# Optimization experiments

Hardware: AMD Instinct MI355X
Metric: run time of the kernel (lower is better)

## Reference

```python
import jax, jax.numpy as jnp
import numpy as np

D_MODEL = 1024
N_HEADS = 16
D_HEAD = D_MODEL // N_HEADS
B, L = 4, 2048
NEG_INF = float('-inf')


def setup_inputs() -> dict:
    key = jax.random.key(0)
    ks = jax.random.split(key, 8)
    x = jax.random.normal(ks[0], (B, L, D_MODEL), dtype=jnp.float32)
    # sorted cumulative event times in hours (~0-2000h span)
    timestamps = jnp.cumsum(jax.random.uniform(ks[1], (B, L), dtype=jnp.float32), axis=-1)
    mask = jnp.ones((B, L), dtype=jnp.float32)
    s = 1.0 / np.sqrt(D_MODEL)
    W_qkv = jax.random.normal(ks[2], (3 * D_MODEL, D_MODEL), dtype=jnp.float32) * s
    b_qkv = jnp.zeros((3 * D_MODEL,), dtype=jnp.float32)
    W_out = jax.random.normal(ks[3], (D_MODEL, D_MODEL), dtype=jnp.float32) * s
    b_out = jnp.zeros((D_MODEL,), dtype=jnp.float32)
    decay_rate = jnp.full((N_HEADS,), 0.01, dtype=jnp.float32)
    return {"x": x, "timestamps": timestamps, "mask": mask,
            "W_qkv": W_qkv, "b_qkv": b_qkv, "W_out": W_out, "b_out": b_out,
            "decay_rate": decay_rate}


def reference(x, timestamps, mask, W_qkv, b_qkv, W_out, b_out, decay_rate):
    Bb, Ll, Dd = x.shape
    H, dh = N_HEADS, D_HEAD
    scale = dh ** (-0.5)
    qkv = x @ W_qkv.T + b_qkv                     # (B,L,3D)
    qkv = qkv.reshape(Bb, Ll, 3, H, dh).transpose(2, 0, 3, 1, 4)  # (3,B,H,L,dh)
    q, k, v = qkv[0], qkv[1], qkv[2]
    attn = jnp.einsum('bhqd,bhkd->bhqk', q, k) * scale
    t_diff = jnp.abs(timestamps[:, :, None] - timestamps[:, None, :])[:, None]  # (B,1,L,L)
    decay = jax.nn.softplus(decay_rate)[None, :, None, None]                    # (1,H,1,1)
    attn = attn - decay * t_diff / 24.0
    causal = jnp.triu(jnp.ones((Ll, Ll), dtype=bool), k=1)        # (L,L) True above diag
    attn = jnp.where(causal[None, None], NEG_INF, attn)
    pad = (mask == 0.0)[:, None, None, :]                         # (B,1,1,L) True=pad key
    attn = jnp.where(pad, NEG_INF, attn)
    attn = jax.nn.softmax(attn, axis=-1)
    out = jnp.einsum('bhqk,bhkd->bhqd', attn, v)                  # (B,H,L,dh)
    out = out.transpose(0, 2, 1, 3).reshape(Bb, Ll, Dd)
    return out @ W_out.T + b_out
```

## Files before the change

### kernel.cpp

```cpp
#include <hip/hip_runtime.h>
#include <stdint.h>
#include <math.h>

#define B_   4
#define L_   2048
#define H_   16
#define DH_  64
#define DM_  1024

typedef __bf16 bf16;
typedef __attribute__((ext_vector_type(8))) __bf16 bf16x8;
typedef __attribute__((ext_vector_type(4))) float f32x4;
typedef __attribute__((ext_vector_type(4))) int i32x4;
typedef __attribute__((ext_vector_type(4))) short s16x4;
typedef unsigned short u16;
typedef unsigned int u32;
typedef __attribute__((ext_vector_type(2))) unsigned int u32x2;
typedef __attribute__((ext_vector_type(4))) unsigned short u16x4;

typedef unsigned int u32g __attribute__((address_space(1)));
typedef unsigned int u32l __attribute__((address_space(3)));

__device__ __forceinline__ u16 f2bf(float f) {
  return __builtin_bit_cast(u16, (bf16)f);
}

__device__ __forceinline__ float exp2_fast(float x) {
  float r; asm("v_exp_f32 %0, %1" : "=v"(r) : "v"(x)); return r;
}

__device__ __forceinline__ void gload16(const void* g, void* l) {
  __builtin_amdgcn_global_load_lds((const u32g*)g, (u32l*)l, 16, 0, 0);
}

__device__ __forceinline__ f32x4 mfma16(s16x4 a, s16x4 b, f32x4 c) {
#if __has_builtin(__builtin_amdgcn_mfma_f32_16x16x16bf16_1k)
  return __builtin_amdgcn_mfma_f32_16x16x16bf16_1k(a, b, c, 0, 0, 0);
#else
  asm volatile("v_mfma_f32_16x16x16_bf16 %0, %1, %2, %0\n\ts_nop 7\n\ts_nop 2"
               : "+v"(c) : "v"(a), "v"(b));
  return c;
#endif
}

#define NX4 2097152
#define NQ4 786432
#define NO4 262144
__global__ __launch_bounds__(256) void cvt3(const float* __restrict__ x,
                                            const float* __restrict__ wq,
                                            const float* __restrict__ wo,
                                            u16* __restrict__ xb, u16* __restrict__ wqb,
                                            u16* __restrict__ wob) {
  int i = blockIdx.x * 256 + threadIdx.x;
  const float* src; u16* dst; int j;
  if (i < NX4)            { src = x;  dst = xb;  j = i; }
  else if (i < NX4 + NQ4) { src = wq; dst = wqb; j = i - NX4; }
  else                    { src = wo; dst = wob; j = i - NX4 - NQ4; }
  f32x4 v = ((const f32x4*)src)[j];
  u16x4 o;
  o[0] = f2bf(v[0]); o[1] = f2bf(v[1]); o[2] = f2bf(v[2]); o[3] = f2bf(v[3]);
  ((u16x4*)dst)[j] = o;
}

__global__ __launch_bounds__(256) void bias_fill(const float* __restrict__ ts,
                                                 const float* __restrict__ msk,
                                                 const float* __restrict__ decay,
                                                 float* __restrict__ Bk) {
  int i = blockIdx.x * 256 + threadIdx.x;
  int bh = i >> 11, l = i & (L_ - 1);
  int b = bh >> 4, h = bh & 15;
  float dc24 = log1pf(__expf(decay[h])) * (1.0f / 24.0f) * 1.44269504f;
  float tv = ts[b * L_ + l], mv = msk[b * L_ + l];
  Bk[i] = (mv != 0.f) ? dc24 * tv : -INFINITY;
}

__global__ __launch_bounds__(512) void gemm_bf16(
    const u16* __restrict__ A, const u16* __restrict__ Bm, const float* __restrict__ bias,
    int M, int N, int K, int mode,
    u16* __restrict__ Qb, u16* __restrict__ Kb, u16* __restrict__ Vt, float* __restrict__ Cout)
{
  __shared__ char smem[147456];
  u16* ltr = (u16*)smem;

  const int tid = threadIdx.x;
  const int nwg = gridDim.x;
  int idx = blockIdx.x;
  idx = (idx & 7) * (nwg >> 3) + (idx >> 3);
  const int nbx = N >> 7;
  const int bx = idx % nbx, by = idx / nbx;
  const int m0 = by << 8, n0 = bx << 7;

  const int lane = tid & 63, w = tid >> 6;
  const int g = lane >> 4, col = lane & 15;
  const int wr = w >> 1, wc = w & 1;

  f32x4 acc[4][4];
#pragma unroll
  for (int mt = 0; mt < 4; ++mt)
#pragma unroll
    for (int nt = 0; nt < 4; ++nt) {
      acc[mt][nt][0] = 0.f; acc[mt][nt][1] = 0.f;
      acc[mt][nt][2] = 0.f; acc[mt][nt][3] = 0.f;
    }

  auto STAGE_A = [&](int kt, int nb, int hh) {
    char* dA = smem + nb * 49152;
    const int k0 = kt << 6;
#pragma unroll
    for (int pp = hh * 2; pp < hh * 2 + 2; ++pp) {
      int c = tid + pp * 512;
      int row = c >> 3, cc = c & 7;
      gload16(A + (size_t)(m0 + row) * K + k0 + ((cc ^ (row & 7)) << 3), dA + c * 16);
    }
  };
  auto STAGE_B = [&](int kt, int nb) {
    char* dB = smem + nb * 49152 + 32768;
    const int k0 = kt << 6;
#pragma unroll
    for (int pp = 0; pp < 2; ++pp) {
      int c = tid + pp * 512;
      int row = c >> 3, cc = c & 7;
      gload16(Bm + (size_t)(n0 + row) * K + k0 + ((cc ^ (row & 7)) << 3), dB + c * 16);
    }
  };

  STAGE_A(0, 0, 0); STAGE_A(0, 0, 1); STAGE_B(0, 0);
  STAGE_A(1, 1, 0); STAGE_A(1, 1, 1); STAGE_B(1, 1);
  asm volatile("s_waitcnt vmcnt(6)" ::: "memory");
  __builtin_amdgcn_s_barrier();

  const int nk = K >> 6;
  for (int t = 0; t < nk; ++t) {
    const char* bufA = smem + (t % 3) * 49152;
    const char* bufB = bufA + 32768;
    const bool pf = (t + 2 < nk);
    const int nb2 = (t + 2) % 3;

    bf16x8 af[4][2], bfr[4][2];
    auto RDA = [&](int mt, int kk) {
      int row = wr * 64 + mt * 16 + col;
      return *(const bf16x8*)(bufA + row * 128 + ((((kk << 2) + g) ^ (row & 7)) << 4));
    };
    auto RDB = [&](int nt, int kk) {
      int row = wc * 64 + nt * 16 + col;
      return *(const bf16x8*)(bufB + row * 128 + ((((kk << 2) + g) ^ (row & 7)) << 4));
    };
    auto QUAD = [&](int qm, int qn) {
      __builtin_amdgcn_s_setprio(1);
#pragma unroll
      for (int mi = 0; mi < 2; ++mi)
#pragma unroll
        for (int ni = 0; ni < 2; ++ni)
#pragma unroll
          for (int kk = 0; kk < 2; ++kk)
            acc[qm * 2 + mi][qn * 2 + ni] = __builtin_amdgcn_mfma_f32_16x16x32_bf16(
                af[qm * 2 + mi][kk], bfr[qn * 2 + ni][kk], acc[qm * 2 + mi][qn * 2 + ni], 0, 0, 0);
      __builtin_amdgcn_s_setprio(0);
    };

#pragma unroll
    for (int mi = 0; mi < 2; ++mi) { af[mi][0] = RDA(mi, 0); af[mi][1] = RDA(mi, 1); }
#pragma unroll
    for (int ni = 0; ni < 2; ++ni) { bfr[ni][0] = RDB(ni, 0); bfr[ni][1] = RDB(ni, 1); }
    if (pf) STAGE_A(t + 2, nb2, 0);
    __builtin_amdgcn_s_barrier();
    asm volatile("s_waitcnt lgkmcnt(0)" ::: "memory");
    __builtin_amdgcn_sched_barrier(0);
    QUAD(0, 0);
    __builtin_amdgcn_s_barrier();

#pragma unroll
    for (int ni = 2; ni < 4; ++ni) { bfr[ni][0] = RDB(ni, 0); bfr[ni][1] = RDB(ni, 1); }
    if (pf) STAGE_A(t + 2, nb2, 1);
    __builtin_amdgcn_s_barrier();
    asm volatile("s_waitcnt lgkmcnt(0)" ::: "memory");
    __builtin_amdgcn_sched_barrier(0);
    QUAD(0, 1);
    __builtin_amdgcn_s_barrier();

#pragma unroll
    for (int mi = 2; mi < 4; ++mi) { af[mi][0] = RDA(mi, 0); af[mi][1] = RDA(mi, 1); }
    if (pf) STAGE_B(t + 2, nb2);
    __builtin_amdgcn_s_barrier();
    asm volatile("s_waitcnt lgkmcnt(0)" ::: "memory");
    __builtin_amdgcn_sched_barrier(0);
    QUAD(1, 1);
    __builtin_amdgcn_s_barrier();

    QUAD(1, 0);
    if (pf)              asm volatile("s_waitcnt vmcnt(6)" ::: "memory");
    else if (t + 1 < nk) asm volatile("s_waitcnt vmcnt(0)" ::: "memory");
    __builtin_amdgcn_s_barrier();
  }

  if (mode == 1) {
#pragma unroll
    for (int nt = 0; nt < 4; ++nt) {
      int gn = n0 + wc * 64 + nt * 16 + col;
      float bv = bias[gn];
#pragma unroll
      for (int mt = 0; mt < 4; ++mt) {
        int mbase = m0 + wr * 64 + mt * 16 + g * 4;
#pragma unroll
        for (int r = 0; r < 4; ++r)
          Cout[(size_t)(mbase + r) * N + gn] = acc[mt][nt][r] + bv;
      }
    }
    return;
  }

  const int type = n0 >> 10;
  const float qsc = (type == 0) ? 0.125f * 1.44269504f : 1.0f;
#pragma unroll
  for (int nt = 0; nt < 4; ++nt) {
    int nn = wc * 64 + nt * 16 + col;
    float bv = bias[n0 + nn];
#pragma unroll
    for (int mt = 0; mt < 4; ++mt) {
      int mm = wr * 64 + mt * 16 + g * 4;
#pragma unroll
      for (int r = 0; r < 4; ++r) {
        u16 hv = f2bf((acc[mt][nt][r] + bv) * qsc);
        if (type < 2) ltr[(mm + r) * 136 + nn] = hv;
        else          ltr[nn * 264 + (mm + r)] = hv;
      }
    }
  }
  __syncthreads();
  if (type < 2) {
#pragma unroll
    for (int it = 0; it < 8; ++it) {
      int cid = tid + it * 512;
      int rrow = cid >> 4, cc = cid & 15;
      i32x4 v = *(const i32x4*)((const char*)ltr + rrow * 272 + cc * 16);
      int token = m0 + rrow;
      int bb = token >> 11, ll = token & (L_ - 1);
      int gn = n0 + cc * 8;
      int head = (gn & 1023) >> 6, d = gn & 63;
      u16* dst = (type == 0) ? Qb : Kb;
      *(i32x4*)(dst + ((size_t)((bb * H_ + head) * L_ + ll)) * 64 + d) = v;
    }
  } else {
#pragma unroll
    for (int it = 0; it < 8; ++it) {
      int cid = tid + it * 512;
      int rrow = cid >> 5, cc = cid & 31;
      i32x4 v = *(const i32x4*)((const char*)ltr + rrow * 528 + cc * 16);
      int gn = n0 + rrow;
      int head = (gn & 1023) >> 6, d = gn & 63;
      int token0 = m0 + cc * 8;
      int bb = token0 >> 11, ll = token0 & (L_ - 1);
      *(i32x4*)(Vt + ((size_t)((bb * H_ + head) * DH_ + d)) * L_ + ll) = v;
    }
  }
}

__global__ __launch_bounds__(512, 2) void attn_fwd(
    const u16* __restrict__ Qb, const u16* __restrict__ Kb, const u16* __restrict__ Vt,
    const float* __restrict__ Bk, u16* __restrict__ AO)
{
  __shared__ u16 lK[3][64 * 64];
  __shared__ u16 lV[3][64 * 64];

  const int phys = blockIdx.x;
  const int xcd = phys & 7, s = phys >> 3;
  const int bh = xcd * 8 + (s >> 3);
  const int pr = s & 7;
  const int qa = pr, qbt = 15 - pr;
  const int b = bh >> 4, h = bh & 15;

  const int tid = threadIdx.x, w = tid >> 6, lane = tid & 63;
  const int g = lane >> 4, q16 = lane & 15;

  const float* Bkb = Bk + (size_t)bh * L_;

  int kcol[2], vcol[4];
#pragma unroll
  for (int kk = 0; kk < 2; ++kk) kcol[kk] = ((kk * 4 + g) ^ (q16 & 7)) << 4;
#pragma unroll
  for (int t = 0; t < 4; ++t)
    vcol[t] = (((2 * t + (g >> 1)) ^ (q16 & 7)) << 4) + (g & 1) * 8;

  const int nkA = (qa + 1) * 2;
  const int nkB = (qbt + 1) * 2;

  auto STAGE = [&](int gst, int nb) {
    const int kt = (gst < nkA) ? gst : gst - nkA;
    const int kg0 = kt * 64;
    const int r8 = tid >> 3, cc = tid & 7;
    gload16(Kb + ((size_t)bh * L_ + kg0 + r8) * 64 + ((cc ^ (r8 & 7)) * 8),
            (char*)lK[nb] + tid * 16);
    gload16(Vt + ((size_t)(bh * 64 + r8)) * L_ + kg0 + ((cc ^ (r8 & 7)) * 8),
            (char*)lV[nb] + tid * 16);
  };

  auto BODY = [&](bf16x8 (&qf)[2], f32x4 (&o)[4], float& l_r, float mn,
                  int qrow, int kg0, int cur) {
    f32x4 sv[4];
#pragma unroll
    for (int t = 0; t < 4; ++t)
      sv[t] = *(const f32x4*)(Bkb + kg0 + t * 16 + g * 4);

    __builtin_amdgcn_s_setprio(1);
#pragma unroll
    for (int t = 0; t < 4; ++t) {
      const char* krow = (const char*)lK[cur] + t * 2048 + q16 * 128;
#pragma unroll
      for (int kk = 0; kk < 2; ++kk) {
        bf16x8 kf = *(const bf16x8*)(krow + kcol[kk]);
        sv[t] = __builtin_amdgcn_mfma_f32_16x16x32_bf16(kf, qf[kk], sv[t], 0, 0, 0);
      }
    }
    __builtin_amdgcn_s_setprio(0);

    if (kg0 + 63 > qrow) {
      const int qg = qrow + q16;
#pragma unroll
      for (int t = 0; t < 4; ++t)
#pragma unroll
        for (int r = 0; r < 4; ++r)
          sv[t][r] = (kg0 + t * 16 + g * 4 + r <= qg) ? sv[t][r] : -INFINITY;
    }

    float rs = 0.f;
#pragma unroll
    for (int t = 0; t < 4; ++t)
#pragma unroll
      for (int r = 0; r < 4; ++r) {
        float pv = exp2_fast(sv[t][r] - mn);
        sv[t][r] = pv;
        rs += pv;
      }
    l_r += rs;

    s16x4 pf[4];
#pragma unroll
    for (int t = 0; t < 4; ++t) {
      s16x4 pp;
      pp[0] = (short)f2bf(sv[t][0]); pp[1] = (short)f2bf(sv[t][1]);
      pp[2] = (short)f2bf(sv[t][2]); pp[3] = (short)f2bf(sv[t][3]);
      pf[t] = pp;
    }

    __builtin_amdgcn_s_setprio(1);
#pragma unroll
    for (int t = 0; t < 4; ++t) {
      const char* vrow = (const char*)lV[cur] + q16 * 128 + vcol[t];
#pragma unroll
      for (int db = 0; db < 4; ++db) {
        s16x4 vf = *(const s16x4*)(vrow + db * 2048);
        o[db] = mfma16(vf, pf[t], o[db]);
      }
    }
    __builtin_amdgcn_s_setprio(0);
  };

  auto EPI = [&](f32x4 (&o)[4], float l_r, int qt) {
    float lt = l_r + __shfl_xor(l_r, 16);
    lt += __shfl_xor(lt, 32);
    float inv = 1.f / lt;
    u16* dst = AO + ((size_t)(b * L_ + qt * 128 + w * 16 + q16)) * DM_ + h * 64 + g * 4;
#pragma unroll
    for (int db = 0; db < 4; ++db) {
      u32x2 pk;
      pk[0] = (u32)f2bf(o[db][0] * inv) | ((u32)f2bf(o[db][1] * inv) << 16);
      pk[1] = (u32)f2bf(o[db][2] * inv) | ((u32)f2bf(o[db][3] * inv) << 16);
      *(u32x2*)(dst + db * 16) = pk;
    }
  };

  STAGE(0, 0);
  STAGE(1, 1);
  asm volatile("s_waitcnt vmcnt(2) lgkmcnt(0)" ::: "memory");
  __builtin_amdgcn_s_barrier();
  __builtin_amdgcn_sched_barrier(0);

  {
    const int qrow = qa * 128 + w * 16;
    const int mkt = (qrow + 79) >> 6;
    const float mn = Bkb[qrow + q16] + 8.f;
    bf16x8 qf[2];
    {
      const u16* Qr = Qb + ((size_t)bh * L_ + qrow + q16) * 64;
      qf[0] = *(const bf16x8*)(Qr + g * 8);
      qf[1] = *(const bf16x8*)(Qr + 32 + g * 8);
    }
    float l_r = 0.f;
    f32x4 o[4];
#pragma unroll
    for (int db = 0; db < 4; ++db) {
      o[db][0] = 0.f; o[db][1] = 0.f; o[db][2] = 0.f; o[db][3] = 0.f;
    }
    for (int st = 0; st < nkA; ++st) {
      const int cur = st % 3;
      STAGE(st + 2, (st + 2) % 3);
      if (st < mkt) BODY(qf, o, l_r, mn, qrow, st * 64, cur);
      asm volatile("s_waitcnt vmcnt(2) lgkmcnt(0)" ::: "memory");
      __builtin_amdgcn_s_barrier();
      __builtin_amdgcn_sched_barrier(0);
    }
    EPI(o, l_r, qa);
  }

  {
    const int qrow = qbt * 128 + w * 16;
    const int mkt = (qrow + 79) >> 6;
    const float mn = Bkb[qrow + q16] + 8.f;
    bf16x8 qf[2];
    {
      const u16* Qr = Qb + ((size_t)bh * L_ + qrow + q16) * 64;
      qf[0] = *(const bf16x8*)(Qr + g * 8);
      qf[1] = *(const bf16x8*)(Qr + 32 + g * 8);
    }
    float l_r = 0.f;
    f32x4 o[4];
#pragma unroll
    for (int db = 0; db < 4; ++db) {
      o[db][0] = 0.f; o[db][1] = 0.f; o[db][2] = 0.f; o[db][3] = 0.f;
    }
    for (int kt = 0; kt < nkB; ++kt) {
      const int gst = nkA + kt;
      const int cur = gst % 3;
      const bool pf = (kt + 2 < nkB);
      if (pf) STAGE(gst + 2, (gst + 2) % 3);
      if (kt < mkt) BODY(qf, o, l_r, mn, qrow, kt * 64, cur);
      if (kt + 1 < nkB) {
        if (pf) asm volatile("s_waitcnt vmcnt(2) lgkmcnt(0)" ::: "memory");
        else    asm volatile("s_waitcnt vmcnt(0) lgkmcnt(0)" ::: "memory");
        __builtin_amdgcn_s_barrier();
        __builtin_amdgcn_sched_barrier(0);
      }
    }
    EPI(o, l_r, qbt);
  }
}

extern "C" void kernel_launch(void* const* d_in, const int* in_sizes, int n_in,
                              void* d_out, int out_size, void* d_ws, size_t ws_size,
                              hipStream_t stream) {
  const float* x    = (const float*)d_in[0];
  const float* ts   = (const float*)d_in[1];
  const float* mk   = (const float*)d_in[2];
  const float* Wqkv = (const float*)d_in[3];
  const float* bqkv = (const float*)d_in[4];
  const float* Wout = (const float*)d_in[5];
  const float* bout = (const float*)d_in[6];
  const float* dec  = (const float*)d_in[7];
  float* out = (float*)d_out;

  char* ws = (char*)d_ws;
  u16* xbf  = (u16*)(ws + 0);
  u16* wqbf = (u16*)(ws + 16777216);
  u16* wobf = (u16*)(ws + 23068672);
  u16* Qb   = (u16*)(ws + 25165824);
  u16* Kb   = (u16*)(ws + 41943040);
  u16* Vt   = (u16*)(ws + 58720256);
  u16* AO   = (u16*)(ws + 75497472);
  float* Bk = (float*)(ws + 92274688);

  cvt3<<<dim3((NX4 + NQ4 + NO4) / 256), 256, 0, stream>>>(x, Wqkv, Wout, xbf, wqbf, wobf);

  bias_fill<<<dim3(64 * 2048 / 256), 256, 0, stream>>>(ts, mk, dec, Bk);

  gemm_bf16<<<dim3(768), 512, 0, stream>>>(
      xbf, wqbf, bqkv, 8192, 3072, 1024, 0, Qb, Kb, Vt, nullptr);

  attn_fwd<<<dim3(512), 512, 0, stream>>>(Qb, Kb, Vt, Bk, AO);

  gemm_bf16<<<dim3(256), 512, 0, stream>>>(
      AO, wobf, bout, 8192, 1024, 1024, 1, nullptr, nullptr, nullptr, out);
}
```

Baseline: 184.1 us.

## Share K/V tiles between paired query tiles in one fused loop

The kernel used to process two query tiles (qa and 15-qa) one after the other, loading the K/V tiles for the qa range twice. The loop is now merged, so each staged K/V tile feeds both query tiles' QK and PV MFMAs while the shorter tile is active. This cuts global loads and barriers for the overlapping range. In exchange it doubles accumulator and score registers, which may lower occupancy or cause spills.

```diff
diff --git a/kernel.cpp b/kernel.cpp
--- a/kernel.cpp
+++ b/kernel.cpp
@@ -284,8 +284,31 @@
   const int nkA = (qa + 1) * 2;
   const int nkB = (qbt + 1) * 2;
 
-  auto STAGE = [&](int gst, int nb) {
-    const int kt = (gst < nkA) ? gst : gst - nkA;
+  const int qrowA = qa * 128 + w * 16, qrowB = qbt * 128 + w * 16;
+  const int mktA = (qrowA + 79) >> 6;
+  const int mktB = (qrowB + 79) >> 6;
+  const float mnA = Bkb[qrowA + q16] + 8.f;
+  const float mnB = Bkb[qrowB + q16] + 8.f;
+
+  bf16x8 qfA[2], qfB[2];
+  {
+    const u16* Qr = Qb + ((size_t)bh * L_ + qrowA + q16) * 64;
+    qfA[0] = *(const bf16x8*)(Qr + g * 8);
+    qfA[1] = *(const bf16x8*)(Qr + 32 + g * 8);
+    Qr = Qb + ((size_t)bh * L_ + qrowB + q16) * 64;
+    qfB[0] = *(const bf16x8*)(Qr + g * 8);
+    qfB[1] = *(const bf16x8*)(Qr + 32 + g * 8);
+  }
+
+  float lA = 0.f, lB = 0.f;
+  f32x4 oA[4], oB[4];
+#pragma unroll
+  for (int db = 0; db < 4; ++db) {
+    oA[db][0] = 0.f; oA[db][1] = 0.f; oA[db][2] = 0.f; oA[db][3] = 0.f;
+    oB[db][0] = 0.f; oB[db][1] = 0.f; oB[db][2] = 0.f; oB[db][3] = 0.f;
+  }
+
+  auto STAGE = [&](int kt, int nb) {
     const int kg0 = kt * 64;
     const int r8 = tid >> 3, cc = tid & 7;
     gload16(Kb + ((size_t)bh * L_ + kg0 + r8) * 64 + ((cc ^ (r8 & 7)) * 8),
@@ -294,12 +317,15 @@
             (char*)lV[nb] + tid * 16);
   };
 
-  auto BODY = [&](bf16x8 (&qf)[2], f32x4 (&o)[4], float& l_r, float mn,
-                  int qrow, int kg0, int cur) {
-    f32x4 sv[4];
+  auto BODY = [&](bool doA, int kg0, int cur) {
+    f32x4 bk[4];
 #pragma unroll
     for (int t = 0; t < 4; ++t)
-      sv[t] = *(const f32x4*)(Bkb + kg0 + t * 16 + g * 4);
+      bk[t] = *(const f32x4*)(Bkb + kg0 + t * 16 + g * 4);
+
+    f32x4 svA[4], svB[4];
+#pragma unroll
+    for (int t = 0; t < 4; ++t) { if (doA) svA[t] = bk[t]; svB[t] = bk[t]; }
 
     __builtin_amdgcn_s_setprio(1);
 #pragma unroll
@@ -308,38 +334,59 @@
 #pragma unroll
       for (int kk = 0; kk < 2; ++kk) {
         bf16x8 kf = *(const bf16x8*)(krow + kcol[kk]);
-        sv[t] = __builtin_amdgcn_mfma_f32_16x16x32_bf16(kf, qf[kk], sv[t], 0, 0, 0);
+        if (doA) svA[t] = __builtin_amdgcn_mfma_f32_16x16x32_bf16(kf, qfA[kk], svA[t], 0, 0, 0);
+        svB[t] = __builtin_amdgcn_mfma_f32_16x16x32_bf16(kf, qfB[kk], svB[t], 0, 0, 0);
       }
     }
     __builtin_amdgcn_s_setprio(0);
 
-    if (kg0 + 63 > qrow) {
-      const int qg = qrow + q16;
+    if (doA && kg0 + 63 > qrowA) {
+      const int qg = qrowA + q16;
 #pragma unroll
       for (int t = 0; t < 4; ++t)
 #pragma unroll
         for (int r = 0; r < 4; ++r)
-          sv[t][r] = (kg0 + t * 16 + g * 4 + r <= qg) ? sv[t][r] : -INFINITY;
-    }
-
-    float rs = 0.f;
-#pragma unroll
-    for (int t = 0; t < 4; ++t)
-#pragma unroll
-      for (int r = 0; r < 4; ++r) {
-        float pv = exp2_fast(sv[t][r] - mn);
-        sv[t][r] = pv;
-        rs += pv;
-      }
-    l_r += rs;
-
-    s16x4 pf[4];
-#pragma unroll
-    for (int t = 0; t < 4; ++t) {
-      s16x4 pp;
-      pp[0] = (short)f2bf(sv[t][0]); pp[1] = (short)f2bf(sv[t][1]);
-      pp[2] = (short)f2bf(sv[t][2]); pp[3] = (short)f2bf(sv[t][3]);
-      pf[t] = pp;
+          svA[t][r] = (kg0 + t * 16 + g * 4 + r <= qg) ? svA[t][r] : -INFINITY;
+    }
+    if (kg0 + 63 > qrowB) {
+      const int qg = qrowB + q16;
+#pragma unroll
+      for (int t = 0; t < 4; ++t)
+#pragma unroll
+        for (int r = 0; r < 4; ++r)
+          svB[t][r] = (kg0 + t * 16 + g * 4 + r <= qg) ? svB[t][r] : -INFINITY;
+    }
+
+    s16x4 pfA[4], pfB[4];
+    if (doA) {
+      float rs = 0.f;
+#pragma unroll
+      for (int t = 0; t < 4; ++t) {
+        s16x4 pp;
+#pragma unroll
+        for (int r = 0; r < 4; ++r) {
+          float pv = exp2_fast(svA[t][r] - mnA);
+          rs += pv;
+          pp[r] = (short)f2bf(pv);
+        }
+        pfA[t] = pp;
+      }
+      lA += rs;
+    }
+    {
+      float rs = 0.f;
+#pragma unroll
+      for (int t = 0; t < 4; ++t) {
+        s16x4 pp;
+#pragma unroll
+        for (int r = 0; r < 4; ++r) {
+          float pv = exp2_fast(svB[t][r] - mnB);
+          rs += pv;
+          pp[r] = (short)f2bf(pv);
+        }
+        pfB[t] = pp;
+      }
+      lB += rs;
     }
 
     __builtin_amdgcn_s_setprio(1);
@@ -349,7 +396,8 @@
 #pragma unroll
       for (int db = 0; db < 4; ++db) {
         s16x4 vf = *(const s16x4*)(vrow + db * 2048);
-        o[db] = mfma16(vf, pf[t], o[db]);
+        if (doA) oA[db] = mfma16(vf, pfA[t], oA[db]);
+        oB[db] = mfma16(vf, pfB[t], oB[db]);
       }
     }
     __builtin_amdgcn_s_setprio(0);
@@ -375,64 +423,21 @@
   __builtin_amdgcn_s_barrier();
   __builtin_amdgcn_sched_barrier(0);
 
-  {
-    const int qrow = qa * 128 + w * 16;
-    const int mkt = (qrow + 79) >> 6;
-    const float mn = Bkb[qrow + q16] + 8.f;
-    bf16x8 qf[2];
-    {
-      const u16* Qr = Qb + ((size_t)bh * L_ + qrow + q16) * 64;
-      qf[0] = *(const bf16x8*)(Qr + g * 8);
-      qf[1] = *(const bf16x8*)(Qr + 32 + g * 8);
-    }
-    float l_r = 0.f;
-    f32x4 o[4];
-#pragma unroll
-    for (int db = 0; db < 4; ++db) {
-      o[db][0] = 0.f; o[db][1] = 0.f; o[db][2] = 0.f; o[db][3] = 0.f;
-    }
-    for (int st = 0; st < nkA; ++st) {
-      const int cur = st % 3;
-      STAGE(st + 2, (st + 2) % 3);
-      if (st < mkt) BODY(qf, o, l_r, mn, qrow, st * 64, cur);
-      asm volatile("s_waitcnt vmcnt(2) lgkmcnt(0)" ::: "memory");
+  for (int kt = 0; kt < nkB; ++kt) {
+    const int cur = kt % 3;
+    const bool pf = (kt + 2 < nkB);
+    if (pf) STAGE(kt + 2, (kt + 2) % 3);
+    if (kt < mktA)      BODY(true,  kt * 64, cur);
+    else if (kt < mktB) BODY(false, kt * 64, cur);
+    if (kt + 1 < nkB) {
+      if (pf) asm volatile("s_waitcnt vmcnt(2) lgkmcnt(0)" ::: "memory");
+      else    asm volatile("s_waitcnt vmcnt(0) lgkmcnt(0)" ::: "memory");
       __builtin_amdgcn_s_barrier();
       __builtin_amdgcn_sched_barrier(0);
     }
-    EPI(o, l_r, qa);
-  }
-
-  {
-    const int qrow = qbt * 128 + w * 16;
-    const int mkt = (qrow + 79) >> 6;
-    const float mn = Bkb[qrow + q16] + 8.f;
-    bf16x8 qf[2];
-    {
-      const u16* Qr = Qb + ((size_t)bh * L_ + qrow + q16) * 64;
-      qf[0] = *(const bf16x8*)(Qr + g * 8);
-      qf[1] = *(const bf16x8*)(Qr + 32 + g * 8);
-    }
-    float l_r = 0.f;
-    f32x4 o[4];
-#pragma unroll
-    for (int db = 0; db < 4; ++db) {
-      o[db][0] = 0.f; o[db][1] = 0.f; o[db][2] = 0.f; o[db][3] = 0.f;
-    }
-    for (int kt = 0; kt < nkB; ++kt) {
-      const int gst = nkA + kt;
-      const int cur = gst % 3;
-      const bool pf = (kt + 2 < nkB);
-      if (pf) STAGE(gst + 2, (gst + 2) % 3);
-      if (kt < mkt) BODY(qf, o, l_r, mn, qrow, kt * 64, cur);
-      if (kt + 1 < nkB) {
-        if (pf) asm volatile("s_waitcnt vmcnt(2) lgkmcnt(0)" ::: "memory");
-        else    asm volatile("s_waitcnt vmcnt(0) lgkmcnt(0)" ::: "memory");
-        __builtin_amdgcn_s_barrier();
-        __builtin_amdgcn_sched_barrier(0);
-      }
-    }
-    EPI(o, l_r, qbt);
-  }
+  }
+  EPI(oA, lA, qa);
+  EPI(oB, lB, qbt);
 }
 
 extern "C" void kernel_launch(void* const* d_in, const int* in_sizes, int n_in,
```

Measured after the change: 220.8 us. 1.2x slower.

## Add dedicated 256x256-tile QKV GEMM kernel with split pipelined staging

Applied to the files above, without the earlier changes.

Adds a specialized gemm_qkv kernel that uses 256x256 output tiles (8 waves, 128x64 per wave) instead of 256x128, halving the grid to 384 blocks. It double-buffers A/B in LDS, interleaves partial global loads between four MFMA quadrants, and uses setprio around the MFMA bursts. The goal is higher arithmetic intensity and better load/compute overlap for the QKV projection. The generic gemm_bf16 keeps only the output-projection epilogue. Larger tiles raise register pressure and leave fewer blocks to balance across CUs.

```diff
diff --git a/kernel.cpp b/kernel.cpp
--- a/kernel.cpp
+++ b/kernel.cpp
@@ -74,14 +74,190 @@
   Bk[i] = (mv != 0.f) ? dc24 * tv : -INFINITY;
 }
 
+__global__ __launch_bounds__(512) void gemm_qkv(
+    const u16* __restrict__ A, const u16* __restrict__ Bm, const float* __restrict__ bias,
+    u16* __restrict__ Qb, u16* __restrict__ Kb, u16* __restrict__ Vt)
+{
+  __shared__ char smem[135168];
+  u16* ltr = (u16*)smem;
+  const int K = 1024, nk = 16;
+
+  const int tid = threadIdx.x;
+  const int nwg = gridDim.x;
+  int idx = blockIdx.x;
+  idx = (idx & 7) * (nwg >> 3) + (idx >> 3);
+  const int nbx = 12;
+  const int bx = idx % nbx, by = idx / nbx;
+  const int m0 = by << 8, n0 = bx << 8;
+
+  const int lane = tid & 63, w = tid >> 6;
+  const int g = lane >> 4, col = lane & 15;
+  const int wr = w >> 2, wc = w & 3;
+
+  f32x4 acc[8][4];
+#pragma unroll
+  for (int mt = 0; mt < 8; ++mt)
+#pragma unroll
+    for (int nt = 0; nt < 4; ++nt) {
+      acc[mt][nt][0] = 0.f; acc[mt][nt][1] = 0.f;
+      acc[mt][nt][2] = 0.f; acc[mt][nt][3] = 0.f;
+    }
+
+  auto SA = [&](int kt, int nb, int q) {
+    char* dA = smem + (nb << 16);
+    int c = (q << 9) + tid;
+    int row = c >> 3, cc = c & 7;
+    gload16(A + (size_t)(m0 + row) * K + (kt << 6) + ((cc ^ (row & 7)) << 3), dA + c * 16);
+  };
+  auto SB = [&](int kt, int nb, int q) {
+    char* dB = smem + (nb << 16) + 32768;
+    int c = (q << 9) + tid;
+    int row = c >> 3, cc = c & 7;
+    gload16(Bm + (size_t)(n0 + row) * K + (kt << 6) + ((cc ^ (row & 7)) << 3), dB + c * 16);
+  };
+
+  SA(0, 0, 0); SA(0, 0, 1); SA(0, 0, 2); SA(0, 0, 3);
+  SB(0, 0, 0); SB(0, 0, 1); SB(0, 0, 2); SB(0, 0, 3);
+  SA(1, 1, 0); SA(1, 1, 2); SB(1, 1, 0); SB(1, 1, 1); SA(1, 1, 1); SA(1, 1, 3);
+  asm volatile("s_waitcnt vmcnt(6)" ::: "memory");
+  __builtin_amdgcn_s_barrier();
+
+  for (int t = 0; t < nk; ++t) {
+    const char* bufA = smem + ((t & 1) << 16);
+    const char* bufB = bufA + 32768;
+    const int nbN = (t + 1) & 1;
+
+    auto RDA = [&](int mt, int kk) {
+      int row = wr * 128 + mt * 16 + col;
+      return *(const bf16x8*)(bufA + row * 128 + ((((kk << 2) + g) ^ (row & 7)) << 4));
+    };
+    auto RDB = [&](int nt, int kk) {
+      int row = wc * 64 + nt * 16 + col;
+      return *(const bf16x8*)(bufB + row * 128 + ((((kk << 2) + g) ^ (row & 7)) << 4));
+    };
+
+    bf16x8 af[4][2], bfr[4][2];
+
+#pragma unroll
+    for (int mi = 0; mi < 4; ++mi) { af[mi][0] = RDA(mi, 0); af[mi][1] = RDA(mi, 1); }
+#pragma unroll
+    for (int ni = 0; ni < 2; ++ni) { bfr[ni][0] = RDB(ni, 0); bfr[ni][1] = RDB(ni, 1); }
+    if (t + 1 < nk) { SB(t + 1, nbN, 2); SB(t + 1, nbN, 3); }
+    __builtin_amdgcn_s_barrier();
+    asm volatile("s_waitcnt lgkmcnt(0)" ::: "memory");
+    __builtin_amdgcn_sched_barrier(0);
+    __builtin_amdgcn_s_setprio(1);
+#pragma unroll
+    for (int mi = 0; mi < 4; ++mi)
+#pragma unroll
+      for (int ni = 0; ni < 2; ++ni)
+#pragma unroll
+        for (int kk = 0; kk < 2; ++kk)
+          acc[mi][ni] = __builtin_amdgcn_mfma_f32_16x16x32_bf16(af[mi][kk], bfr[ni][kk], acc[mi][ni], 0, 0, 0);
+    __builtin_amdgcn_s_setprio(0);
+    __builtin_amdgcn_s_barrier();
+
+#pragma unroll
+    for (int ni = 2; ni < 4; ++ni) { bfr[ni][0] = RDB(ni, 0); bfr[ni][1] = RDB(ni, 1); }
+    if (t + 2 < nk) { SA(t + 2, t & 1, 0); SA(t + 2, t & 1, 2); }
+    __builtin_amdgcn_s_barrier();
+    asm volatile("s_waitcnt lgkmcnt(0)" ::: "memory");
+    __builtin_amdgcn_sched_barrier(0);
+    __builtin_amdgcn_s_setprio(1);
+#pragma unroll
+    for (int mi = 0; mi < 4; ++mi)
+#pragma unroll
+      for (int ni = 2; ni < 4; ++ni)
+#pragma unroll
+        for (int kk = 0; kk < 2; ++kk)
+          acc[mi][ni] = __builtin_amdgcn_mfma_f32_16x16x32_bf16(af[mi][kk], bfr[ni][kk], acc[mi][ni], 0, 0, 0);
+    __builtin_amdgcn_s_setprio(0);
+    __builtin_amdgcn_s_barrier();
+
+#pragma unroll
+    for (int mi = 0; mi < 4; ++mi) { af[mi][0] = RDA(mi + 4, 0); af[mi][1] = RDA(mi + 4, 1); }
+    if (t + 2 < nk) { SB(t + 2, t & 1, 0); SB(t + 2, t & 1, 1); }
+    __builtin_amdgcn_s_barrier();
+    asm volatile("s_waitcnt lgkmcnt(0)" ::: "memory");
+    __builtin_amdgcn_sched_barrier(0);
+    __builtin_amdgcn_s_setprio(1);
+#pragma unroll
+    for (int mi = 0; mi < 4; ++mi)
+#pragma unroll
+      for (int ni = 2; ni < 4; ++ni)
+#pragma unroll
+        for (int kk = 0; kk < 2; ++kk)
+          acc[mi + 4][ni] = __builtin_amdgcn_mfma_f32_16x16x32_bf16(af[mi][kk], bfr[ni][kk], acc[mi + 4][ni], 0, 0, 0);
+    __builtin_amdgcn_s_setprio(0);
+    __builtin_amdgcn_s_barrier();
+
+    if (t + 2 < nk) { SA(t + 2, t & 1, 1); SA(t + 2, t & 1, 3); }
+    __builtin_amdgcn_s_setprio(1);
+#pragma unroll
+    for (int mi = 0; mi < 4; ++mi)
+#pragma unroll
+      for (int ni = 0; ni < 2; ++ni)
+#pragma unroll
+        for (int kk = 0; kk < 2; ++kk)
+          acc[mi + 4][ni] = __builtin_amdgcn_mfma_f32_16x16x32_bf16(af[mi][kk], bfr[ni][kk], acc[mi + 4][ni], 0, 0, 0);
+    __builtin_amdgcn_s_setprio(0);
+    if (t + 2 < nk) asm volatile("s_waitcnt vmcnt(6)" ::: "memory");
+    else            asm volatile("s_waitcnt vmcnt(0)" ::: "memory");
+    __builtin_amdgcn_s_barrier();
+  }
+
+  const int type = n0 >> 10;
+  const float qsc = (type == 0) ? 0.125f * 1.44269504f : 1.0f;
+#pragma unroll
+  for (int nt = 0; nt < 4; ++nt) {
+    int nn = wc * 64 + nt * 16 + col;
+    float bv = bias[n0 + nn];
+#pragma unroll
+    for (int mt = 0; mt < 8; ++mt) {
+      int mm = wr * 128 + mt * 16 + g * 4;
+#pragma unroll
+      for (int r = 0; r < 4; ++r) {
+        u16 hv = f2bf((acc[mt][nt][r] + bv) * qsc);
+        if (type < 2) ltr[(mm + r) * 264 + nn] = hv;
+        else          ltr[nn * 264 + (mm + r)] = hv;
+      }
+    }
+  }
+  __syncthreads();
+  if (type < 2) {
+#pragma unroll
+    for (int it = 0; it < 16; ++it) {
+      int cid = tid + it * 512;
+      int rrow = cid >> 5, cc = cid & 31;
+      i32x4 v = *(const i32x4*)((const char*)ltr + rrow * 528 + cc * 16);
+      int token = m0 + rrow;
+      int bb = token >> 11, ll = token & (L_ - 1);
+      int gn = n0 + cc * 8;
+      int head = (gn & 1023) >> 6, d = gn & 63;
+      u16* dst = (type == 0) ? Qb : Kb;
+      *(i32x4*)(dst + ((size_t)((bb * H_ + head) * L_ + ll)) * 64 + d) = v;
+    }
+  } else {
+#pragma unroll
+    for (int it = 0; it < 16; ++it) {
+      int cid = tid + it * 512;
+      int rrow = cid >> 5, cc = cid & 31;
+      i32x4 v = *(const i32x4*)((const char*)ltr + rrow * 528 + cc * 16);
+      int gn = n0 + rrow;
+      int head = (gn & 1023) >> 6, d = gn & 63;
+      int token0 = m0 + cc * 8;
+      int bb = token0 >> 11, ll = token0 & (L_ - 1);
+      *(i32x4*)(Vt + ((size_t)((bb * H_ + head) * DH_ + d)) * L_ + ll) = v;
+    }
+  }
+}
+
 __global__ __launch_bounds__(512) void gemm_bf16(
     const u16* __restrict__ A, const u16* __restrict__ Bm, const float* __restrict__ bias,
     int M, int N, int K, int mode,
     u16* __restrict__ Qb, u16* __restrict__ Kb, u16* __restrict__ Vt, float* __restrict__ Cout)
 {
   __shared__ char smem[147456];
-  u16* ltr = (u16*)smem;
-
   const int tid = threadIdx.x;
   const int nwg = gridDim.x;
   int idx = blockIdx.x;
@@ -193,64 +369,16 @@
     __builtin_amdgcn_s_barrier();
   }
 
-  if (mode == 1) {
-#pragma unroll
-    for (int nt = 0; nt < 4; ++nt) {
-      int gn = n0 + wc * 64 + nt * 16 + col;
-      float bv = bias[gn];
-#pragma unroll
-      for (int mt = 0; mt < 4; ++mt) {
-        int mbase = m0 + wr * 64 + mt * 16 + g * 4;
-#pragma unroll
-        for (int r = 0; r < 4; ++r)
-          Cout[(size_t)(mbase + r) * N + gn] = acc[mt][nt][r] + bv;
-      }
-    }
-    return;
-  }
-
-  const int type = n0 >> 10;
-  const float qsc = (type == 0) ? 0.125f * 1.44269504f : 1.0f;
 #pragma unroll
   for (int nt = 0; nt < 4; ++nt) {
-    int nn = wc * 64 + nt * 16 + col;
-    float bv = bias[n0 + nn];
+    int gn = n0 + wc * 64 + nt * 16 + col;
+    float bv = bias[gn];
 #pragma unroll
     for (int mt = 0; mt < 4; ++mt) {
-      int mm = wr * 64 + mt * 16 + g * 4;
-#pragma unroll
-      for (int r = 0; r < 4; ++r) {
-        u16 hv = f2bf((acc[mt][nt][r] + bv) * qsc);
-        if (type < 2) ltr[(mm + r) * 136 + nn] = hv;
-        else          ltr[nn * 264 + (mm + r)] = hv;
-      }
-    }
-  }
-  __syncthreads();
-  if (type < 2) {
-#pragma unroll
-    for (int it = 0; it < 8; ++it) {
-      int cid = tid + it * 512;
-      int rrow = cid >> 4, cc = cid & 15;
-      i32x4 v = *(const i32x4*)((const char*)ltr + rrow * 272 + cc * 16);
-      int token = m0 + rrow;
-      int bb = token >> 11, ll = token & (L_ - 1);
-      int gn = n0 + cc * 8;
-      int head = (gn & 1023) >> 6, d = gn & 63;
-      u16* dst = (type == 0) ? Qb : Kb;
-      *(i32x4*)(dst + ((size_t)((bb * H_ + head) * L_ + ll)) * 64 + d) = v;
-    }
-  } else {
-#pragma unroll
-    for (int it = 0; it < 8; ++it) {
-      int cid = tid + it * 512;
-      int rrow = cid >> 5, cc = cid & 31;
-      i32x4 v = *(const i32x4*)((const char*)ltr + rrow * 528 + cc * 16);
-      int gn = n0 + rrow;
-      int head = (gn & 1023) >> 6, d = gn & 63;
-      int token0 = m0 + cc * 8;
-      int bb = token0 >> 11, ll = token0 & (L_ - 1);
-      *(i32x4*)(Vt + ((size_t)((bb * H_ + head) * DH_ + d)) * L_ + ll) = v;
+      int mbase = m0 + wr * 64 + mt * 16 + g * 4;
+#pragma unroll
+      for (int r = 0; r < 4; ++r)
+        Cout[(size_t)(mbase + r) * N + gn] = acc[mt][nt][r] + bv;
     }
   }
 }
@@ -462,8 +590,7 @@
 
   bias_fill<<<dim3(64 * 2048 / 256), 256, 0, stream>>>(ts, mk, dec, Bk);
 
-  gemm_bf16<<<dim3(768), 512, 0, stream>>>(
-      xbf, wqbf, bqkv, 8192, 3072, 1024, 0, Qb, Kb, Vt, nullptr);
+  gemm_qkv<<<dim3(384), 512, 0, stream>>>(xbf, wqbf, bqkv, Qb, Kb, Vt);
 
   attn_fwd<<<dim3(512), 512, 0, stream>>>(Qb, Kb, Vt, Bk, AO);
 
```

Result: faster. 174.4 us (-5.3%).
